# Performance work log

Measured on AMD Instinct MI355X. Metric: run time of the kernel, lower is better.

Reference implementation:

```python
import jax, jax.numpy as jnp
import numpy as np

LN_EPS = 1e-5
N_HEAD_CHANNELS = 32  # model_dim=256 -> 8 heads


def _layer_norm(x, g, b):
    m = jnp.mean(x, axis=-1, keepdims=True)
    v = jnp.mean((x - m) ** 2, axis=-1, keepdims=True)
    return (x - m) * jax.lax.rsqrt(v + LN_EPS) * g + b


def setup_inputs() -> dict:
    key = jax.random.key(0)
    ks = jax.random.split(key, 12)
    b, n, nv, f = 1, 65536, 1, 256
    s = 256  # 4 ** seq_level_attention
    w = 0.02
    d = {}
    d["x"] = jax.random.normal(ks[0], (b, n, nv, f), jnp.float32)
    d["mask"] = jnp.ones((b, n, nv), dtype=bool)
    d["pos_embeddings"] = jax.random.normal(ks[1], (nv, s, f), jnp.float32) * w
    d["W_emb"] = jax.random.normal(ks[2], (f, 2 * f), jnp.float32) * w
    d["b_emb"] = jnp.zeros((2 * f,), jnp.float32)
    d["ln1_g"] = jnp.ones((f,), jnp.float32)
    d["ln1_b"] = jnp.zeros((f,), jnp.float32)
    d["Wq"] = jax.random.normal(ks[3], (f, f), jnp.float32) * w
    d["bq"] = jnp.zeros((f,), jnp.float32)
    d["Wk"] = jax.random.normal(ks[4], (f, f), jnp.float32) * w
    d["bk"] = jnp.zeros((f,), jnp.float32)
    d["Wv"] = jax.random.normal(ks[5], (f, f), jnp.float32) * w
    d["bv"] = jnp.zeros((f,), jnp.float32)
    d["Wo"] = jax.random.normal(ks[6], (f, f), jnp.float32) * w
    d["bo"] = jnp.zeros((f,), jnp.float32)
    d["ln2_g"] = jnp.ones((f,), jnp.float32)
    d["ln2_b"] = jnp.zeros((f,), jnp.float32)
    d["W1"] = jax.random.normal(ks[7], (f, f), jnp.float32) * w
    d["W2"] = jax.random.normal(ks[8], (f, f), jnp.float32) * w
    d["gamma"] = jnp.ones((f,), jnp.float32) * 1e-6
    d["gamma_mlp"] = jnp.ones((f,), jnp.float32) * 1e-6
    return d


def reference(x, mask, pos_embeddings, W_emb, b_emb, ln1_g, ln1_b,
              Wq, bq, Wk, bk, Wv, bv, Wo, bo, ln2_g, ln2_b, W1, W2,
              gamma, gamma_mlp):
    b, n, nv, f = x.shape
    s = pos_embeddings.shape[1]          # window length = 4**seq_level
    n_seq = n // s
    n_heads = f // N_HEAD_CHANNELS
    hd = f // n_heads

    x_res = x
    # sequenize: (b, n, nv, f) -> (b, n_seq, s, nv, f)
    xs = x.reshape(b, n_seq, s, nv, f)
    ms = mask.reshape(b, n_seq, s, nv)
    # mask_update: a vertex stays valid only if its whole window is valid
    mask_update = (ms & jnp.all(ms, axis=-2, keepdims=True)).reshape(b, n, nv)

    # shift/scale from position embeddings: (nv, s, 2f) -> (s, nv, 2f)
    emb = jnp.swapaxes(pos_embeddings @ W_emb + b_emb, -2, -3)
    shift, scale = jnp.split(emb, 2, axis=-1)  # each (s, nv, f)

    xm = _layer_norm(xs, ln1_g, ln1_b) * (scale + 1.0) + shift

    B = b * n_seq
    L = s * nv
    xf = xm.reshape(B, L, f)
    mf = ms.reshape(B, L)

    def heads(t):
        return t.reshape(B, L, n_heads, hd).transpose(0, 2, 1, 3)

    q = heads(xf @ Wq + bq)
    k = heads(xf @ Wk + bk)
    v = heads(xf @ Wv + bv)

    scores = jnp.einsum('bhqd,bhkd->bhqk', q, k) / np.sqrt(hd).astype(np.float32)
    scores = scores + jnp.where(mf[:, None, None, :], 0.0, -1e9)
    attn = jax.nn.softmax(scores, axis=-1)
    out = jnp.einsum('bhqk,bhkd->bhqd', attn, v)
    out = out.transpose(0, 2, 1, 3).reshape(B, L, f) @ Wo + bo

    x = x_res + gamma * out.reshape(b, n, nv, f)
    h = _layer_norm(x, ln2_g, ln2_b) @ W1
    h = jax.nn.silu(h) @ W2
    x = x + gamma_mlp * h
    return (x, mask_update)
```

## Files before the change

kernel.cpp:

```cpp
#include <hip/hip_runtime.h>
#include <cstddef>
#include <cstdint>

typedef unsigned short u16;
typedef short s16x8 __attribute__((ext_vector_type(8)));
typedef float f32x4 __attribute__((ext_vector_type(4)));
typedef int   i32x4 __attribute__((ext_vector_type(4)));
typedef u16   u16x4 __attribute__((ext_vector_type(4)));

__device__ __forceinline__ float b2f(u16 u) {
  union { unsigned int i; float f; } v; v.i = ((unsigned int)u) << 16; return v.f;
}
__device__ __forceinline__ u16 f2b(float f) {
  union { float f; unsigned int i; } v; v.f = f;
  unsigned int r = v.i + 0x7fffu + ((v.i >> 16) & 1u);
  return (u16)(r >> 16);
}
__device__ __forceinline__ unsigned int cvt_pk(float a, float b) {
  unsigned int r;
  asm("v_cvt_pk_bf16_f32 %0, %1, %2" : "=v"(r) : "v"(a), "v"(b));
  return r;
}

__global__ __launch_bounds__(256) void transpose6(
    const float* __restrict__ w0, const float* __restrict__ w1,
    const float* __restrict__ w2, const float* __restrict__ w3,
    const float* __restrict__ w4, const float* __restrict__ w5,
    u16* __restrict__ wt)
{
  __shared__ u16 T[64][66];
  const float* src;
  switch (blockIdx.x) {
    case 0: src = w0; break; case 1: src = w1; break;
    case 2: src = w2; break; case 3: src = w3; break;
    case 4: src = w4; break; default: src = w5; break;
  }
  u16* dst = wt + (size_t)blockIdx.x * 65536;
  const int tr = (blockIdx.y & 3) * 64;
  const int tc = (blockIdx.y >> 2) * 64;
  const int lane = threadIdx.x & 63, grp = threadIdx.x >> 6;
  #pragma unroll
  for (int i = 0; i < 16; ++i) {
    const int r = grp + i * 4;
    T[lane][r] = f2b(src[(size_t)(tr + r) * 256 + tc + lane]);
  }
  __syncthreads();
  #pragma unroll
  for (int i = 0; i < 16; ++i) {
    const int j = grp + i * 4;
    dst[(size_t)(tc + j) * 256 + tr + lane] = T[j][lane];
  }
}

__global__ __launch_bounds__(256) void film_kernel(
    const float* __restrict__ pos, const float* __restrict__ Wemb,
    const float* __restrict__ bemb, float* __restrict__ shift,
    float* __restrict__ scale)
{
  __shared__ float prow[256];
  __shared__ float psum[4][64];
  const int s = blockIdx.x, t = threadIdx.x;
  const int ks = t >> 6, cl = t & 63;
  const int c = blockIdx.y * 64 + cl;
  prow[t] = pos[s * 256 + t];
  __syncthreads();
  float acc = 0.f;
  #pragma unroll 8
  for (int kk = ks * 64; kk < ks * 64 + 64; ++kk)
    acc = fmaf(prow[kk], Wemb[kk * 512 + c], acc);
  psum[ks][cl] = acc;
  __syncthreads();
  if (t < 64) {
    const int cc = blockIdx.y * 64 + t;
    const float v = psum[0][t] + psum[1][t] + psum[2][t] + psum[3][t] + bemb[cc];
    if (cc < 256) shift[s * 256 + cc] = v;
    else          scale[s * 256 + cc - 256] = v;
  }
}

__global__ __launch_bounds__(256) void ln_kernel(
    const float* __restrict__ xf, const u16* __restrict__ xb,
    const float* __restrict__ shift, const float* __restrict__ scale,
    const float* __restrict__ g, const float* __restrict__ b,
    u16* __restrict__ out)
{
  const int lane = threadIdx.x & 63;
  const int l = lane & 15, grp = lane >> 4;
  const int token = blockIdx.x * 16 + (threadIdx.x >> 6) * 4 + grp;
  const size_t tb = (size_t)token * 256;
  const int spos = token & 255;

  if (xf) {
    f32x4 v[4];
    #pragma unroll
    for (int j = 0; j < 4; ++j) v[j] = *(const f32x4*)(xf + tb + 4 * l + 64 * j);
    float s = 0.f, s2 = 0.f;
    #pragma unroll
    for (int j = 0; j < 4; ++j)
      #pragma unroll
      for (int i = 0; i < 4; ++i) { s += v[j][i]; s2 += v[j][i] * v[j][i]; }
    #pragma unroll
    for (int off = 8; off >= 1; off >>= 1) {
      s  += __shfl_xor(s, off);
      s2 += __shfl_xor(s2, off);
    }
    const float mean = s * 0.00390625f;
    const float inv  = rsqrtf(s2 * 0.00390625f - mean * mean + 1e-5f);
    #pragma unroll
    for (int j = 0; j < 4; ++j) {
      const int e = 4 * l + 64 * j;
      const f32x4 gv = *(const f32x4*)(g + e);
      const f32x4 bv = *(const f32x4*)(b + e);
      f32x4 sc = {0.f,0.f,0.f,0.f}, sh = {0.f,0.f,0.f,0.f};
      if (shift) {
        sc = *(const f32x4*)(scale + spos * 256 + e);
        sh = *(const f32x4*)(shift + spos * 256 + e);
      }
      u16x4 o;
      #pragma unroll
      for (int i = 0; i < 4; ++i) {
        float ln = (v[j][i] - mean) * inv * gv[i] + bv[i];
        if (shift) ln = ln * (sc[i] + 1.0f) + sh[i];
        o[i] = f2b(ln);
      }
      *(u16x4*)(out + tb + e) = o;
    }
  } else {
    s16x8 r[2];
    #pragma unroll
    for (int j = 0; j < 2; ++j) r[j] = *(const s16x8*)(xb + tb + 8 * l + 128 * j);
    float v[2][8];
    float s = 0.f, s2 = 0.f;
    #pragma unroll
    for (int j = 0; j < 2; ++j)
      #pragma unroll
      for (int i = 0; i < 8; ++i) {
        const float f = b2f((u16)r[j][i]);
        v[j][i] = f; s += f; s2 += f * f;
      }
    #pragma unroll
    for (int off = 8; off >= 1; off >>= 1) {
      s  += __shfl_xor(s, off);
      s2 += __shfl_xor(s2, off);
    }
    const float mean = s * 0.00390625f;
    const float inv  = rsqrtf(s2 * 0.00390625f - mean * mean + 1e-5f);
    #pragma unroll
    for (int j = 0; j < 2; ++j) {
      const int e = 8 * l + 128 * j;
      const f32x4 g0 = *(const f32x4*)(g + e);
      const f32x4 g1 = *(const f32x4*)(g + e + 4);
      const f32x4 b0 = *(const f32x4*)(b + e);
      const f32x4 b1 = *(const f32x4*)(b + e + 4);
      s16x8 o;
      #pragma unroll
      for (int i = 0; i < 4; ++i) {
        o[i]     = (short)f2b((v[j][i]     - mean) * inv * g0[i] + b0[i]);
        o[i + 4] = (short)f2b((v[j][i + 4] - mean) * inv * g1[i] + b1[i]);
      }
      *(s16x8*)(out + tb + e) = o;
    }
  }
}

__global__ __launch_bounds__(256) void gemm_qkv(
    const u16* __restrict__ A, const u16* __restrict__ wt,
    const float* __restrict__ bq, const float* __restrict__ bk,
    const float* __restrict__ bv, u16* __restrict__ qo,
    u16* __restrict__ ko, u16* __restrict__ vo)
{
  __shared__ __align__(16) u16 Alds[128][72];
  __shared__ __align__(16) u16 Blds[128][72];
  const int bid = blockIdx.x;
  const int xcd = bid & 7, rr = bid >> 3;
  const int xx = rr % 6;
  const int yy = (rr / 6) * 8 + xcd;
  const int wsel = xx >> 1;
  const int m0 = yy * 128;
  const int n0 = (xx & 1) * 128;
  const u16* BT = wt + (size_t)wsel * 65536;
  const int t = threadIdx.x;
  const int wave = t >> 6, lane = t & 63;
  const int wm = (wave & 1) * 64, wn = (wave >> 1) * 64;
  const int lrow = lane & 15, lk = (lane >> 4) * 8;

  f32x4 acc[4][4];
  #pragma unroll
  for (int i = 0; i < 4; ++i)
    #pragma unroll
    for (int j = 0; j < 4; ++j)
      acc[i][j] = f32x4{0.f, 0.f, 0.f, 0.f};

  for (int k0 = 0; k0 < 256; k0 += 64) {
    #pragma unroll
    for (int i = 0; i < 4; ++i) {
      const int c = i * 256 + t;
      const int row = c >> 3, col = (c & 7) * 8;
      *(i32x4*)(&Alds[row][col]) = *(const i32x4*)(A  + (size_t)(m0 + row) * 256 + k0 + col);
      *(i32x4*)(&Blds[row][col]) = *(const i32x4*)(BT + (size_t)(n0 + row) * 256 + k0 + col);
    }
    __syncthreads();
    #pragma unroll
    for (int kk = 0; kk < 64; kk += 32) {
      s16x8 af[4], bf[4];
      #pragma unroll
      for (int mt = 0; mt < 4; ++mt) af[mt] = *(const s16x8*)(&Alds[wm + mt*16 + lrow][kk + lk]);
      #pragma unroll
      for (int nt = 0; nt < 4; ++nt) bf[nt] = *(const s16x8*)(&Blds[wn + nt*16 + lrow][kk + lk]);
      #pragma unroll
      for (int mt = 0; mt < 4; ++mt)
        #pragma unroll
        for (int nt = 0; nt < 4; ++nt)
          acc[mt][nt] = __builtin_amdgcn_mfma_f32_16x16x32_bf16(af[mt], bf[nt], acc[mt][nt], 0, 0, 0);
    }
    __syncthreads();
  }

  const float* bias = (wsel == 0) ? bq : (wsel == 1) ? bk : bv;
  u16* qko = (wsel == 0) ? qo : ko;
  #pragma unroll
  for (int mt = 0; mt < 4; ++mt) {
    const int mb = m0 + wm + mt*16 + (lane >> 4) * 4;
    const int w = mb >> 8, tok = mb & 255;
    #pragma unroll
    for (int nt = 0; nt < 4; ++nt) {
      const int n = n0 + wn + nt*16 + lrow;
      const int h = n >> 5, d = n & 31;
      const float bv_ = bias[n];
      if (wsel < 2) {
        #pragma unroll
        for (int r = 0; r < 4; ++r)
          qko[(size_t)w * 65536 + h * 8192 + (tok + r) * 32 + d] = f2b(acc[mt][nt][r] + bv_);
      } else {
        u16x4 pk;
        #pragma unroll
        for (int r = 0; r < 4; ++r) pk[r] = f2b(acc[mt][nt][r] + bv_);
        const int vaddr = ((tok >> 5) << 10) + (((tok >> 2) & 3) << 8)
                        + d * 8 + (((tok >> 4) & 1) << 2);
        *(u16x4*)(vo + (size_t)w * 65536 + h * 8192 + vaddr) = pk;
      }
    }
  }
}

__global__ __launch_bounds__(256) void gemm256(
    const u16* __restrict__ A, const u16* __restrict__ BT,
    const float* __restrict__ bias, const float* __restrict__ extra_f,
    const u16* __restrict__ extra_b, const float* __restrict__ coef,
    u16* __restrict__ out_b, float* __restrict__ out_f, int mode)
{
  __shared__ __align__(16) u16 Alds[128][72];
  __shared__ __align__(16) u16 Blds[128][72];
  const int bid = blockIdx.x;
  const int xcd = bid & 7, rr = bid >> 3;
  const int n0 = (rr & 1) * 128;
  const int m0 = ((rr >> 1) * 8 + xcd) * 128;
  const int t = threadIdx.x;
  const int wave = t >> 6, lane = t & 63;
  const int wm = (wave & 1) * 64, wn = (wave >> 1) * 64;
  const int lrow = lane & 15, lk = (lane >> 4) * 8;

  f32x4 acc[4][4];
  #pragma unroll
  for (int i = 0; i < 4; ++i)
    #pragma unroll
    for (int j = 0; j < 4; ++j)
      acc[i][j] = f32x4{0.f, 0.f, 0.f, 0.f};

  for (int k0 = 0; k0 < 256; k0 += 64) {
    #pragma unroll
    for (int i = 0; i < 4; ++i) {
      const int c = i * 256 + t;
      const int row = c >> 3, col = (c & 7) * 8;
      *(i32x4*)(&Alds[row][col]) = *(const i32x4*)(A  + (size_t)(m0 + row) * 256 + k0 + col);
      *(i32x4*)(&Blds[row][col]) = *(const i32x4*)(BT + (size_t)(n0 + row) * 256 + k0 + col);
    }
    __syncthreads();
    #pragma unroll
    for (int kk = 0; kk < 64; kk += 32) {
      s16x8 af[4], bf[4];
      #pragma unroll
      for (int mt = 0; mt < 4; ++mt) af[mt] = *(const s16x8*)(&Alds[wm + mt*16 + lrow][kk + lk]);
      #pragma unroll
      for (int nt = 0; nt < 4; ++nt) bf[nt] = *(const s16x8*)(&Blds[wn + nt*16 + lrow][kk + lk]);
      #pragma unroll
      for (int mt = 0; mt < 4; ++mt)
        #pragma unroll
        for (int nt = 0; nt < 4; ++nt)
          acc[mt][nt] = __builtin_amdgcn_mfma_f32_16x16x32_bf16(af[mt], bf[nt], acc[mt][nt], 0, 0, 0);
    }
    __syncthreads();
  }

  #pragma unroll
  for (int mt = 0; mt < 4; ++mt) {
    const int mb = m0 + wm + mt*16 + (lane >> 4) * 4;
    #pragma unroll
    for (int nt = 0; nt < 4; ++nt) {
      const int n = n0 + wn + nt*16 + lrow;
      const float bv = bias ? bias[n] : 0.0f;
      #pragma unroll
      for (int r = 0; r < 4; ++r) {
        const int m = mb + r;
        const size_t oi = (size_t)m * 256 + n;
        const float y = acc[mt][nt][r] + bv;
        if (mode == 2)      out_b[oi] = f2b(extra_f[oi] + coef[n] * y);
        else if (mode == 3) out_b[oi] = f2b(y / (1.0f + __expf(-y)));
        else                out_f[oi] = b2f(extra_b[oi]) + coef[n] * y;
      }
    }
  }
}

__global__ __launch_bounds__(512) void gemm_mlp(
    const u16* __restrict__ A, const u16* __restrict__ W1T,
    const u16* __restrict__ W2T, const u16* __restrict__ x1,
    const float* __restrict__ gml, float* __restrict__ outx)
{
  __shared__ __align__(16) u16 Blds[256][72];
  __shared__ __align__(16) u16 Hlds[64][264];
  const int m0 = blockIdx.x * 64;
  const int t = threadIdx.x;
  const int wave = t >> 6, lane = t & 63;
  const int wm = (wave & 1) * 32, wn = (wave >> 1) * 64;
  const int lrow = lane & 15, lk = (lane >> 4) * 8;
  const int quad = lane >> 4, col = lane & 15;

  f32x4 acc[2][4];
  #pragma unroll
  for (int i = 0; i < 2; ++i)
    #pragma unroll
    for (int j = 0; j < 4; ++j) acc[i][j] = f32x4{0.f,0.f,0.f,0.f};

  for (int p = 0; p < 4; ++p) {
    const int k0 = p * 64;
    #pragma unroll
    for (int i = 0; i < 4; ++i) {
      const int bb = i * 8192 + t * 16;
      const int n = bb >> 7, kk = (bb & 127) >> 1;
      *(i32x4*)(&Blds[n][kk]) = *(const i32x4*)(W1T + (size_t)n * 256 + k0 + kk);
    }
    __syncthreads();
    #pragma unroll
    for (int kk = 0; kk < 64; kk += 32) {
      s16x8 af[2], bf[4];
      #pragma unroll
      for (int mt = 0; mt < 2; ++mt)
        af[mt] = *(const s16x8*)(A + (size_t)(m0 + wm + mt*16 + lrow) * 256 + k0 + kk + lk);
      #pragma unroll
      for (int nt = 0; nt < 4; ++nt)
        bf[nt] = *(const s16x8*)(&Blds[wn + nt*16 + lrow][kk + lk]);
      #pragma unroll
      for (int mt = 0; mt < 2; ++mt)
        #pragma unroll
        for (int nt = 0; nt < 4; ++nt)
          acc[mt][nt] = __builtin_amdgcn_mfma_f32_16x16x32_bf16(af[mt], bf[nt], acc[mt][nt], 0, 0, 0);
    }
    __syncthreads();
  }

  #pragma unroll
  for (int mt = 0; mt < 2; ++mt)
    #pragma unroll
    for (int nt = 0; nt < 4; ++nt)
      #pragma unroll
      for (int r = 0; r < 4; ++r) {
        const float y = acc[mt][nt][r];
        const float hsig = __builtin_amdgcn_rcpf(1.0f + __builtin_amdgcn_exp2f(-1.442695041f * y));
        Hlds[wm + mt*16 + quad*4 + r][wn + nt*16 + col] = f2b(y * hsig);
        acc[mt][nt][r] = 0.0f;
      }
  __syncthreads();

  for (int p = 0; p < 4; ++p) {
    const int k0 = p * 64;
    #pragma unroll
    for (int i = 0; i < 4; ++i) {
      const int bb = i * 8192 + t * 16;
      const int n = bb >> 7, kk = (bb & 127) >> 1;
      *(i32x4*)(&Blds[n][kk]) = *(const i32x4*)(W2T + (size_t)n * 256 + k0 + kk);
    }
    __syncthreads();
    #pragma unroll
    for (int kk = 0; kk < 64; kk += 32) {
      s16x8 af[2], bf[4];
      #pragma unroll
      for (int mt = 0; mt < 2; ++mt)
        af[mt] = *(const s16x8*)(&Hlds[wm + mt*16 + lrow][k0 + kk + lk]);
      #pragma unroll
      for (int nt = 0; nt < 4; ++nt)
        bf[nt] = *(const s16x8*)(&Blds[wn + nt*16 + lrow][kk + lk]);
      #pragma unroll
      for (int mt = 0; mt < 2; ++mt)
        #pragma unroll
        for (int nt = 0; nt < 4; ++nt)
          acc[mt][nt] = __builtin_amdgcn_mfma_f32_16x16x32_bf16(af[mt], bf[nt], acc[mt][nt], 0, 0, 0);
    }
    __syncthreads();
  }

  #pragma unroll
  for (int mt = 0; mt < 2; ++mt) {
    const int mb = m0 + wm + mt*16 + quad*4;
    #pragma unroll
    for (int nt = 0; nt < 4; ++nt) {
      const int n = wn + nt*16 + col;
      const float gn = gml[n];
      #pragma unroll
      for (int r = 0; r < 4; ++r) {
        const size_t oi = (size_t)(mb + r) * 256 + n;
        outx[oi] = b2f(x1[oi]) + gn * acc[mt][nt][r];
      }
    }
  }
}

__global__ __launch_bounds__(512) void attn256(
    const u16* __restrict__ q, const u16* __restrict__ k,
    const u16* __restrict__ vt, const float* __restrict__ fbias,
    u16* __restrict__ out)
{
  __shared__ __align__(16) u16 KV[16384];
  __shared__ __align__(16) u16 OB[8][16][40];
  const int bid = blockIdx.x;
  const int xcd = bid & 7, rr = bid >> 3;
  const int q0 = (rr & 1) * 128;
  const int s_ = (rr >> 1) * 8 + xcd;
  const int h = s_ & 7, w = s_ >> 3;
  const int t = threadIdx.x;
  const int wave = t >> 6, lane = t & 63;
  const int col = lane & 15, quad = lane >> 4;
  const size_t hb = (size_t)w * 65536 + (size_t)h * 8192;
  const int qr0 = q0 + wave * 16;
  const float sc2 = 0.25508586f;

  {
    const char* kg = (const char*)(k + hb);
    const char* vg = (const char*)(vt + hb);
    const i32x4 r0 = *(const i32x4*)(kg + t * 16);
    const i32x4 r1 = *(const i32x4*)(kg + 8192 + t * 16);
    const i32x4 r2 = *(const i32x4*)(vg + t * 16);
    const i32x4 r3 = *(const i32x4*)(vg + 8192 + t * 16);
    char* lb = (char*)KV;
    *(i32x4*)(lb + t * 16)         = r0;
    *(i32x4*)(lb + 8192 + t * 16)  = r1;
    *(i32x4*)(lb + 16384 + t * 16) = r2;
    *(i32x4*)(lb + 24576 + t * 16) = r3;
  }

  const s16x8 af = *(const s16x8*)(q + hb + (qr0 + col) * 32 + quad * 8);
  const float* fbb = fbias + w * 256 + quad * 4;
  __syncthreads();

  f32x4 acc[16];
  #pragma unroll
  for (int tl = 0; tl < 16; ++tl) {
    const s16x8 kf = *(const s16x8*)(KV + (tl * 16 + col) * 32 + quad * 8);
    acc[tl] = __builtin_amdgcn_mfma_f32_16x16x32_bf16(kf, af, f32x4{0.f,0.f,0.f,0.f}, 0, 0, 0);
  }

  #pragma unroll
  for (int tl = 0; tl < 16; ++tl) {
    const f32x4 fb = *(const f32x4*)(fbb + tl * 16);
    #pragma unroll
    for (int r = 0; r < 4; ++r)
      acc[tl][r] = fmaf(acc[tl][r], sc2, fb[r]);
  }

  f32x4 m4 = acc[0];
  #pragma unroll
  for (int tl = 1; tl < 16; ++tl)
    #pragma unroll
    for (int r = 0; r < 4; ++r)
      m4[r] = fmaxf(m4[r], acc[tl][r]);
  float mx = fmaxf(fmaxf(m4[0], m4[1]), fmaxf(m4[2], m4[3]));
  mx = fmaxf(mx, __shfl_xor(mx, 16));
  mx = fmaxf(mx, __shfl_xor(mx, 32));

  f32x4 s4 = {0.f, 0.f, 0.f, 0.f};
  #pragma unroll
  for (int tl = 0; tl < 16; ++tl) {
    #pragma unroll
    for (int r = 0; r < 4; ++r) {
      const float e = __builtin_amdgcn_exp2f(acc[tl][r] - mx);
      acc[tl][r] = e;
      s4[r] += e;
    }
  }
  float sum = (s4[0] + s4[1]) + (s4[2] + s4[3]);
  sum += __shfl_xor(sum, 16);
  sum += __shfl_xor(sum, 32);
  const float inv = __builtin_amdgcn_rcpf(sum);

  f32x4 o0 = {0.f,0.f,0.f,0.f}, o1 = {0.f,0.f,0.f,0.f};
  const u16* vl = KV + 8192;
  #pragma unroll
  for (int s = 0; s < 8; ++s) {
    i32x4 pi;
    pi[0] = (int)cvt_pk(acc[2*s][0],     acc[2*s][1]);
    pi[1] = (int)cvt_pk(acc[2*s][2],     acc[2*s][3]);
    pi[2] = (int)cvt_pk(acc[2*s + 1][0], acc[2*s + 1][1]);
    pi[3] = (int)cvt_pk(acc[2*s + 1][2], acc[2*s + 1][3]);
    const s16x8 pf = *(const s16x8*)&pi;
    const s16x8 vf0 = *(const s16x8*)(vl + s * 1024 + quad * 256 + col * 8);
    const s16x8 vf1 = *(const s16x8*)(vl + s * 1024 + quad * 256 + col * 8 + 128);
    o0 = __builtin_amdgcn_mfma_f32_16x16x32_bf16(pf, vf0, o0, 0, 0, 0);
    o1 = __builtin_amdgcn_mfma_f32_16x16x32_bf16(pf, vf1, o1, 0, 0, 0);
  }

  f32x4 invr;
  #pragma unroll
  for (int r = 0; r < 4; ++r) invr[r] = __shfl(inv, quad * 4 + r);

  #pragma unroll
  for (int r = 0; r < 4; ++r) {
    OB[wave][quad * 4 + r][col]      = f2b(o0[r] * invr[r]);
    OB[wave][quad * 4 + r][col + 16] = f2b(o1[r] * invr[r]);
  }
  const s16x8 ov = *(const s16x8*)(&OB[wave][col][quad * 8]);
  *(s16x8*)(out + (size_t)w * 65536 + (size_t)(qr0 + col) * 256 + h * 32 + quad * 8) = ov;
}

__global__ __launch_bounds__(256) void maskup(const int* __restrict__ mask,
                                              float* __restrict__ out,
                                              float* __restrict__ fbias)
{
  __shared__ int wall[4];
  const int w = blockIdx.x, t = threadIdx.x;
  const int v = (mask[w * 256 + t] != 0) ? 1 : 0;
  const int a = __all(v);
  if ((t & 63) == 0) wall[t >> 6] = a;
  __syncthreads();
  const int allw = wall[0] & wall[1] & wall[2] & wall[3];
  out[w * 256 + t] = (v & allw) ? 1.0f : 0.0f;
  fbias[w * 256 + t] = v ? 0.0f : -1.0e9f;
}

extern "C" void kernel_launch(void* const* d_in, const int* in_sizes, int n_in,
                              void* d_out, int out_size, void* d_ws, size_t ws_size,
                              hipStream_t stream)
{
  (void)in_sizes; (void)n_in; (void)out_size; (void)ws_size;
  const float* x    = (const float*)d_in[0];
  const int*   mask = (const int*)d_in[1];
  const float* pos  = (const float*)d_in[2];
  const float* Wemb = (const float*)d_in[3];
  const float* bemb = (const float*)d_in[4];
  const float* ln1g = (const float*)d_in[5];
  const float* ln1b = (const float*)d_in[6];
  const float* Wq   = (const float*)d_in[7];
  const float* bq   = (const float*)d_in[8];
  const float* Wk   = (const float*)d_in[9];
  const float* bk   = (const float*)d_in[10];
  const float* Wv   = (const float*)d_in[11];
  const float* bv   = (const float*)d_in[12];
  const float* Wo   = (const float*)d_in[13];
  const float* bo   = (const float*)d_in[14];
  const float* ln2g = (const float*)d_in[15];
  const float* ln2b = (const float*)d_in[16];
  const float* W1   = (const float*)d_in[17];
  const float* W2   = (const float*)d_in[18];
  const float* gam  = (const float*)d_in[19];
  const float* gml  = (const float*)d_in[20];

  char* ws = (char*)d_ws;
  float* shift = (float*)ws;
  float* scale = (float*)(ws + (256 << 10));
  u16*   wt    = (u16*)(ws + (512 << 10));
  float* fbias = (float*)(ws + (1280 << 10));
  u16*   b0    = (u16*)(ws + ((size_t)2  << 20));
  u16*   b1    = (u16*)(ws + ((size_t)34 << 20));
  u16*   b2    = (u16*)(ws + ((size_t)66 << 20));
  u16*   b3    = (u16*)(ws + ((size_t)98 << 20));
  float* outx  = (float*)d_out;
  float* outm  = outx + 16777216;

  const u16* WoT = wt + 3 * 65536;
  const u16* W1T = wt + 4 * 65536;
  const u16* W2T = wt + 5 * 65536;

  transpose6<<<dim3(6, 16), 256, 0, stream>>>(Wq, Wk, Wv, Wo, W1, W2, wt);
  film_kernel<<<dim3(256, 8), 256, 0, stream>>>(pos, Wemb, bemb, shift, scale);
  maskup<<<256, 256, 0, stream>>>(mask, outm, fbias);
  ln_kernel<<<4096, 256, 0, stream>>>(x, nullptr, shift, scale, ln1g, ln1b, b0);
  gemm_qkv<<<3072, 256, 0, stream>>>(b0, wt, bq, bk, bv, b1, b2, b3);
  attn256<<<4096, 512, 0, stream>>>(b1, b2, b3, fbias, b0);
  gemm256<<<1024, 256, 0, stream>>>(b0, WoT, bo, x, nullptr, gam, b1, nullptr, 2);
  ln_kernel<<<4096, 256, 0, stream>>>(nullptr, b1, nullptr, nullptr, ln2g, ln2b, b2);
  gemm_mlp<<<1024, 512, 0, stream>>>(b2, W1T, W2T, b1, gml, outx);
}
```

Baseline: 375.0 us.

## Fuse output projection, residual, LayerNorm2 and MLP into one tail kernel

Replaces the separate Wo GEMM, the second LayerNorm kernel and the MLP kernel with a single kernel. Each block of 64 rows computes the Wo projection plus residual, keeps the bf16-rounded x1 in registers, reduces LayerNorm statistics through shared memory, writes the normalized rows into LDS, then runs W1, SiLU and W2. This removes the global round trips of x1 and the LN output and two launches. In exchange the Wo GEMM now uses the MLP kernel's 64-row tiling, adds extra barriers, and raises register pressure from holding x1 across the MLP.

```diff
diff --git a/kernel.cpp b/kernel.cpp
--- a/kernel.cpp
+++ b/kernel.cpp
@@ -79,7 +79,7 @@
 }
 
 __global__ __launch_bounds__(256) void ln_kernel(
-    const float* __restrict__ xf, const u16* __restrict__ xb,
+    const float* __restrict__ xf,
     const float* __restrict__ shift, const float* __restrict__ scale,
     const float* __restrict__ g, const float* __restrict__ b,
     u16* __restrict__ out)
@@ -90,76 +90,36 @@
   const size_t tb = (size_t)token * 256;
   const int spos = token & 255;
 
-  if (xf) {
-    f32x4 v[4];
-    #pragma unroll
-    for (int j = 0; j < 4; ++j) v[j] = *(const f32x4*)(xf + tb + 4 * l + 64 * j);
-    float s = 0.f, s2 = 0.f;
-    #pragma unroll
-    for (int j = 0; j < 4; ++j)
-      #pragma unroll
-      for (int i = 0; i < 4; ++i) { s += v[j][i]; s2 += v[j][i] * v[j][i]; }
-    #pragma unroll
-    for (int off = 8; off >= 1; off >>= 1) {
-      s  += __shfl_xor(s, off);
-      s2 += __shfl_xor(s2, off);
-    }
-    const float mean = s * 0.00390625f;
-    const float inv  = rsqrtf(s2 * 0.00390625f - mean * mean + 1e-5f);
-    #pragma unroll
-    for (int j = 0; j < 4; ++j) {
-      const int e = 4 * l + 64 * j;
-      const f32x4 gv = *(const f32x4*)(g + e);
-      const f32x4 bv = *(const f32x4*)(b + e);
-      f32x4 sc = {0.f,0.f,0.f,0.f}, sh = {0.f,0.f,0.f,0.f};
-      if (shift) {
-        sc = *(const f32x4*)(scale + spos * 256 + e);
-        sh = *(const f32x4*)(shift + spos * 256 + e);
-      }
-      u16x4 o;
-      #pragma unroll
-      for (int i = 0; i < 4; ++i) {
-        float ln = (v[j][i] - mean) * inv * gv[i] + bv[i];
-        if (shift) ln = ln * (sc[i] + 1.0f) + sh[i];
-        o[i] = f2b(ln);
-      }
-      *(u16x4*)(out + tb + e) = o;
-    }
-  } else {
-    s16x8 r[2];
-    #pragma unroll
-    for (int j = 0; j < 2; ++j) r[j] = *(const s16x8*)(xb + tb + 8 * l + 128 * j);
-    float v[2][8];
-    float s = 0.f, s2 = 0.f;
-    #pragma unroll
-    for (int j = 0; j < 2; ++j)
-      #pragma unroll
-      for (int i = 0; i < 8; ++i) {
-        const float f = b2f((u16)r[j][i]);
-        v[j][i] = f; s += f; s2 += f * f;
-      }
-    #pragma unroll
-    for (int off = 8; off >= 1; off >>= 1) {
-      s  += __shfl_xor(s, off);
-      s2 += __shfl_xor(s2, off);
-    }
-    const float mean = s * 0.00390625f;
-    const float inv  = rsqrtf(s2 * 0.00390625f - mean * mean + 1e-5f);
-    #pragma unroll
-    for (int j = 0; j < 2; ++j) {
-      const int e = 8 * l + 128 * j;
-      const f32x4 g0 = *(const f32x4*)(g + e);
-      const f32x4 g1 = *(const f32x4*)(g + e + 4);
-      const f32x4 b0 = *(const f32x4*)(b + e);
-      const f32x4 b1 = *(const f32x4*)(b + e + 4);
-      s16x8 o;
-      #pragma unroll
-      for (int i = 0; i < 4; ++i) {
-        o[i]     = (short)f2b((v[j][i]     - mean) * inv * g0[i] + b0[i]);
-        o[i + 4] = (short)f2b((v[j][i + 4] - mean) * inv * g1[i] + b1[i]);
-      }
-      *(s16x8*)(out + tb + e) = o;
-    }
+  f32x4 v[4];
+  #pragma unroll
+  for (int j = 0; j < 4; ++j) v[j] = *(const f32x4*)(xf + tb + 4 * l + 64 * j);
+  float s = 0.f, s2 = 0.f;
+  #pragma unroll
+  for (int j = 0; j < 4; ++j)
+    #pragma unroll
+    for (int i = 0; i < 4; ++i) { s += v[j][i]; s2 += v[j][i] * v[j][i]; }
+  #pragma unroll
+  for (int off = 8; off >= 1; off >>= 1) {
+    s  += __shfl_xor(s, off);
+    s2 += __shfl_xor(s2, off);
+  }
+  const float mean = s * 0.00390625f;
+  const float inv  = rsqrtf(s2 * 0.00390625f - mean * mean + 1e-5f);
+  #pragma unroll
+  for (int j = 0; j < 4; ++j) {
+    const int e = 4 * l + 64 * j;
+    const f32x4 gv = *(const f32x4*)(g + e);
+    const f32x4 bv = *(const f32x4*)(b + e);
+    const f32x4 sc = *(const f32x4*)(scale + spos * 256 + e);
+    const f32x4 sh = *(const f32x4*)(shift + spos * 256 + e);
+    u16x4 o;
+    #pragma unroll
+    for (int i = 0; i < 4; ++i) {
+      float ln = (v[j][i] - mean) * inv * gv[i] + bv[i];
+      ln = ln * (sc[i] + 1.0f) + sh[i];
+      o[i] = f2b(ln);
+    }
+    *(u16x4*)(out + tb + e) = o;
   }
 }
 
@@ -243,82 +203,18 @@
   }
 }
 
-__global__ __launch_bounds__(256) void gemm256(
-    const u16* __restrict__ A, const u16* __restrict__ BT,
-    const float* __restrict__ bias, const float* __restrict__ extra_f,
-    const u16* __restrict__ extra_b, const float* __restrict__ coef,
-    u16* __restrict__ out_b, float* __restrict__ out_f, int mode)
-{
-  __shared__ __align__(16) u16 Alds[128][72];
-  __shared__ __align__(16) u16 Blds[128][72];
-  const int bid = blockIdx.x;
-  const int xcd = bid & 7, rr = bid >> 3;
-  const int n0 = (rr & 1) * 128;
-  const int m0 = ((rr >> 1) * 8 + xcd) * 128;
-  const int t = threadIdx.x;
-  const int wave = t >> 6, lane = t & 63;
-  const int wm = (wave & 1) * 64, wn = (wave >> 1) * 64;
-  const int lrow = lane & 15, lk = (lane >> 4) * 8;
-
-  f32x4 acc[4][4];
-  #pragma unroll
-  for (int i = 0; i < 4; ++i)
-    #pragma unroll
-    for (int j = 0; j < 4; ++j)
-      acc[i][j] = f32x4{0.f, 0.f, 0.f, 0.f};
-
-  for (int k0 = 0; k0 < 256; k0 += 64) {
-    #pragma unroll
-    for (int i = 0; i < 4; ++i) {
-      const int c = i * 256 + t;
-      const int row = c >> 3, col = (c & 7) * 8;
-      *(i32x4*)(&Alds[row][col]) = *(const i32x4*)(A  + (size_t)(m0 + row) * 256 + k0 + col);
-      *(i32x4*)(&Blds[row][col]) = *(const i32x4*)(BT + (size_t)(n0 + row) * 256 + k0 + col);
-    }
-    __syncthreads();
-    #pragma unroll
-    for (int kk = 0; kk < 64; kk += 32) {
-      s16x8 af[4], bf[4];
-      #pragma unroll
-      for (int mt = 0; mt < 4; ++mt) af[mt] = *(const s16x8*)(&Alds[wm + mt*16 + lrow][kk + lk]);
-      #pragma unroll
-      for (int nt = 0; nt < 4; ++nt) bf[nt] = *(const s16x8*)(&Blds[wn + nt*16 + lrow][kk + lk]);
-      #pragma unroll
-      for (int mt = 0; mt < 4; ++mt)
-        #pragma unroll
-        for (int nt = 0; nt < 4; ++nt)
-          acc[mt][nt] = __builtin_amdgcn_mfma_f32_16x16x32_bf16(af[mt], bf[nt], acc[mt][nt], 0, 0, 0);
-    }
-    __syncthreads();
-  }
-
-  #pragma unroll
-  for (int mt = 0; mt < 4; ++mt) {
-    const int mb = m0 + wm + mt*16 + (lane >> 4) * 4;
-    #pragma unroll
-    for (int nt = 0; nt < 4; ++nt) {
-      const int n = n0 + wn + nt*16 + lrow;
-      const float bv = bias ? bias[n] : 0.0f;
-      #pragma unroll
-      for (int r = 0; r < 4; ++r) {
-        const int m = mb + r;
-        const size_t oi = (size_t)m * 256 + n;
-        const float y = acc[mt][nt][r] + bv;
-        if (mode == 2)      out_b[oi] = f2b(extra_f[oi] + coef[n] * y);
-        else if (mode == 3) out_b[oi] = f2b(y / (1.0f + __expf(-y)));
-        else                out_f[oi] = b2f(extra_b[oi]) + coef[n] * y;
-      }
-    }
-  }
-}
-
-__global__ __launch_bounds__(512) void gemm_mlp(
-    const u16* __restrict__ A, const u16* __restrict__ W1T,
-    const u16* __restrict__ W2T, const u16* __restrict__ x1,
-    const float* __restrict__ gml, float* __restrict__ outx)
+__global__ __launch_bounds__(512) void gemm_tail(
+    const u16* __restrict__ A, const u16* __restrict__ WoT,
+    const u16* __restrict__ W1T, const u16* __restrict__ W2T,
+    const float* __restrict__ bo, const float* __restrict__ x,
+    const float* __restrict__ gam, const float* __restrict__ lg2,
+    const float* __restrict__ lb2, const float* __restrict__ gml,
+    float* __restrict__ outx)
 {
   __shared__ __align__(16) u16 Blds[256][72];
-  __shared__ __align__(16) u16 Hlds[64][264];
+  __shared__ __align__(16) u16 XH[64][264];
+  __shared__ float LNp[4][64][2];
+  __shared__ float LNm[64][2];
   const int m0 = blockIdx.x * 64;
   const int t = threadIdx.x;
   const int wave = t >> 6, lane = t & 63;
@@ -338,7 +234,7 @@
     for (int i = 0; i < 4; ++i) {
       const int bb = i * 8192 + t * 16;
       const int n = bb >> 7, kk = (bb & 127) >> 1;
-      *(i32x4*)(&Blds[n][kk]) = *(const i32x4*)(W1T + (size_t)n * 256 + k0 + kk);
+      *(i32x4*)(&Blds[n][kk]) = *(const i32x4*)(WoT + (size_t)n * 256 + k0 + kk);
     }
     __syncthreads();
     #pragma unroll
@@ -359,6 +255,117 @@
     __syncthreads();
   }
 
+  unsigned int x1p[2][4][2];
+  float s[2][4], s2[2][4];
+  #pragma unroll
+  for (int mt = 0; mt < 2; ++mt)
+    #pragma unroll
+    for (int r = 0; r < 4; ++r) { s[mt][r] = 0.f; s2[mt][r] = 0.f; }
+
+  #pragma unroll
+  for (int mt = 0; mt < 2; ++mt) {
+    const int mb = m0 + wm + mt*16 + quad*4;
+    #pragma unroll
+    for (int nt = 0; nt < 4; ++nt) {
+      const int n = wn + nt*16 + col;
+      const float bon = bo[n], gn = gam[n];
+      float v[4];
+      #pragma unroll
+      for (int r = 0; r < 4; ++r)
+        v[r] = x[(size_t)(mb + r) * 256 + n] + gn * (acc[mt][nt][r] + bon);
+      const unsigned int p0 = cvt_pk(v[0], v[1]);
+      const unsigned int p1 = cvt_pk(v[2], v[3]);
+      x1p[mt][nt][0] = p0;
+      x1p[mt][nt][1] = p1;
+      const float r0 = b2f((u16)(p0 & 0xffffu)), r1 = b2f((u16)(p0 >> 16));
+      const float r2 = b2f((u16)(p1 & 0xffffu)), r3 = b2f((u16)(p1 >> 16));
+      s[mt][0] += r0; s2[mt][0] += r0 * r0;
+      s[mt][1] += r1; s2[mt][1] += r1 * r1;
+      s[mt][2] += r2; s2[mt][2] += r2 * r2;
+      s[mt][3] += r3; s2[mt][3] += r3 * r3;
+    }
+  }
+  #pragma unroll
+  for (int off = 1; off <= 8; off <<= 1) {
+    #pragma unroll
+    for (int mt = 0; mt < 2; ++mt)
+      #pragma unroll
+      for (int r = 0; r < 4; ++r) {
+        s[mt][r]  += __shfl_xor(s[mt][r],  off);
+        s2[mt][r] += __shfl_xor(s2[mt][r], off);
+      }
+  }
+  if (col == 0) {
+    #pragma unroll
+    for (int mt = 0; mt < 2; ++mt)
+      #pragma unroll
+      for (int r = 0; r < 4; ++r) {
+        const int row = wm + mt*16 + quad*4 + r;
+        LNp[wave >> 1][row][0] = s[mt][r];
+        LNp[wave >> 1][row][1] = s2[mt][r];
+      }
+  }
+  __syncthreads();
+  if (t < 64) {
+    const float ss  = LNp[0][t][0] + LNp[1][t][0] + LNp[2][t][0] + LNp[3][t][0];
+    const float ss2 = LNp[0][t][1] + LNp[1][t][1] + LNp[2][t][1] + LNp[3][t][1];
+    const float mean = ss * 0.00390625f;
+    LNm[t][0] = mean;
+    LNm[t][1] = rsqrtf(ss2 * 0.00390625f - mean * mean + 1e-5f);
+  }
+  __syncthreads();
+  #pragma unroll
+  for (int mt = 0; mt < 2; ++mt) {
+    #pragma unroll
+    for (int nt = 0; nt < 4; ++nt) {
+      const int n = wn + nt*16 + col;
+      const float gg = lg2[n], bb_ = lb2[n];
+      #pragma unroll
+      for (int rr = 0; rr < 2; ++rr) {
+        const unsigned int pk = x1p[mt][nt][rr];
+        #pragma unroll
+        for (int h2 = 0; h2 < 2; ++h2) {
+          const int r = rr * 2 + h2;
+          const int row = wm + mt*16 + quad*4 + r;
+          const float rv = b2f((u16)(h2 ? (pk >> 16) : (pk & 0xffffu)));
+          const float xn = (rv - LNm[row][0]) * LNm[row][1] * gg + bb_;
+          XH[row][n] = f2b(xn);
+        }
+      }
+    }
+  }
+  __syncthreads();
+
+  #pragma unroll
+  for (int i = 0; i < 2; ++i)
+    #pragma unroll
+    for (int j = 0; j < 4; ++j) acc[i][j] = f32x4{0.f,0.f,0.f,0.f};
+  for (int p = 0; p < 4; ++p) {
+    const int k0 = p * 64;
+    #pragma unroll
+    for (int i = 0; i < 4; ++i) {
+      const int bb = i * 8192 + t * 16;
+      const int n = bb >> 7, kk = (bb & 127) >> 1;
+      *(i32x4*)(&Blds[n][kk]) = *(const i32x4*)(W1T + (size_t)n * 256 + k0 + kk);
+    }
+    __syncthreads();
+    #pragma unroll
+    for (int kk = 0; kk < 64; kk += 32) {
+      s16x8 af[2], bf[4];
+      #pragma unroll
+      for (int mt = 0; mt < 2; ++mt)
+        af[mt] = *(const s16x8*)(&XH[wm + mt*16 + lrow][k0 + kk + lk]);
+      #pragma unroll
+      for (int nt = 0; nt < 4; ++nt)
+        bf[nt] = *(const s16x8*)(&Blds[wn + nt*16 + lrow][kk + lk]);
+      #pragma unroll
+      for (int mt = 0; mt < 2; ++mt)
+        #pragma unroll
+        for (int nt = 0; nt < 4; ++nt)
+          acc[mt][nt] = __builtin_amdgcn_mfma_f32_16x16x32_bf16(af[mt], bf[nt], acc[mt][nt], 0, 0, 0);
+    }
+    __syncthreads();
+  }
   #pragma unroll
   for (int mt = 0; mt < 2; ++mt)
     #pragma unroll
@@ -367,7 +374,7 @@
       for (int r = 0; r < 4; ++r) {
         const float y = acc[mt][nt][r];
         const float hsig = __builtin_amdgcn_rcpf(1.0f + __builtin_amdgcn_exp2f(-1.442695041f * y));
-        Hlds[wm + mt*16 + quad*4 + r][wn + nt*16 + col] = f2b(y * hsig);
+        XH[wm + mt*16 + quad*4 + r][wn + nt*16 + col] = f2b(y * hsig);
         acc[mt][nt][r] = 0.0f;
       }
   __syncthreads();
@@ -386,7 +393,7 @@
       s16x8 af[2], bf[4];
       #pragma unroll
       for (int mt = 0; mt < 2; ++mt)
-        af[mt] = *(const s16x8*)(&Hlds[wm + mt*16 + lrow][k0 + kk + lk]);
+        af[mt] = *(const s16x8*)(&XH[wm + mt*16 + lrow][k0 + kk + lk]);
       #pragma unroll
       for (int nt = 0; nt < 4; ++nt)
         bf[nt] = *(const s16x8*)(&Blds[wn + nt*16 + lrow][kk + lk]);
@@ -407,9 +414,10 @@
       const int n = wn + nt*16 + col;
       const float gn = gml[n];
       #pragma unroll
-      for (int r = 0; r < 4; ++r) {
-        const size_t oi = (size_t)(mb + r) * 256 + n;
-        outx[oi] = b2f(x1[oi]) + gn * acc[mt][nt][r];
+      for (int rr = 0; rr < 2; ++rr) {
+        const unsigned int pk = x1p[mt][nt][rr];
+        outx[(size_t)(mb + rr*2    ) * 256 + n] = b2f((u16)(pk & 0xffffu)) + gn * acc[mt][nt][rr*2];
+        outx[(size_t)(mb + rr*2 + 1) * 256 + n] = b2f((u16)(pk >> 16))     + gn * acc[mt][nt][rr*2 + 1];
       }
     }
   }
@@ -582,10 +590,9 @@
   transpose6<<<dim3(6, 16), 256, 0, stream>>>(Wq, Wk, Wv, Wo, W1, W2, wt);
   film_kernel<<<dim3(256, 8), 256, 0, stream>>>(pos, Wemb, bemb, shift, scale);
   maskup<<<256, 256, 0, stream>>>(mask, outm, fbias);
-  ln_kernel<<<4096, 256, 0, stream>>>(x, nullptr, shift, scale, ln1g, ln1b, b0);
+  ln_kernel<<<4096, 256, 0, stream>>>(x, shift, scale, ln1g, ln1b, b0);
   gemm_qkv<<<3072, 256, 0, stream>>>(b0, wt, bq, bk, bv, b1, b2, b3);
   attn256<<<4096, 512, 0, stream>>>(b1, b2, b3, fbias, b0);
-  gemm256<<<1024, 256, 0, stream>>>(b0, WoT, bo, x, nullptr, gam, b1, nullptr, 2);
-  ln_kernel<<<4096, 256, 0, stream>>>(nullptr, b1, nullptr, nullptr, ln2g, ln2b, b2);
-  gemm_mlp<<<1024, 512, 0, stream>>>(b2, W1T, W2T, b1, gml, outx);
-}
+  gemm_tail<<<1024, 512, 0, stream>>>(b0, WoT, W1T, W2T, bo, x, gam,
+                                      ln2g, ln2b, gml, outx);
+}
```

Measured after the change: 348.7 us. 1.08x faster.
